# Kernel tuning notes

Hardware: AMD Instinct MI355X
Metric: run time of the kernel (lower is better)

The kernel has to match this reference:

```python
import jax, jax.numpy as jnp
import numpy as np

B, DIM, H, W = 8, 128, 64, 64
C, DI, N, R, K = DIM // 4, 2 * (DIM // 4), 16, 2, 4  # chunk dim, d_inner, d_state, dt_rank, n_dirs
L = H * W
EPS = 1e-5


def dwconv(x, w, b, dil):
    # x: [B,C,H,W]; w: [C,1,kh,kw] depthwise; torch padding='same' with dilation
    y = jax.lax.conv_general_dilated(
        x, w, window_strides=(1, 1), padding='SAME', rhs_dilation=(dil, dil),
        dimension_numbers=('NCHW', 'OIHW', 'NCHW'), feature_group_count=x.shape[1])
    return y + b[None, :, None, None]


def layernorm(x, w, b):
    mu = jnp.mean(x, -1, keepdims=True)
    var = jnp.var(x, -1, keepdims=True)
    return (x - mu) * jax.lax.rsqrt(var + EPS) * w + b


def axial_dw(x, mh_w, mh_b, mw_w, mw_b, c_w, c_b, dil):
    skip = x
    x = dwconv(x, mw_w, mw_b, dil)   # (1,7) kernel
    x = dwconv(x, mh_w, mh_b, dil)   # (7,1) kernel
    x = dwconv(x, c_w, c_b, dil)     # 3x3 kernel
    return x + skip


def ss2d(x, in_proj_w, conv_w, conv_b, x_proj_w, dt_proj_w, dt_proj_b,
         A_log, D, out_norm_w, out_norm_b, out_proj_w):
    # x: [B,H,W,C] channels-last (VMamba SS2D)
    b, h, w, _ = x.shape
    xz = jnp.einsum('bhwc,ec->bhwe', x, in_proj_w)          # [B,H,W,2*DI]
    xc, z = jnp.split(xz, 2, axis=-1)
    xc = xc.transpose(0, 3, 1, 2)                           # [B,DI,H,W]
    xc = jax.nn.silu(dwconv(xc, conv_w, conv_b, 1))
    l = h * w
    x_hw = xc.reshape(b, DI, l)
    x_wh = xc.transpose(0, 1, 3, 2).reshape(b, DI, l)
    xs = jnp.stack([x_hw, x_wh], 1)                         # [B,2,DI,L]
    xs = jnp.concatenate([xs, jnp.flip(xs, -1)], 1)         # [B,4,DI,L]
    x_dbl = jnp.einsum('bkdl,kcd->bkcl', xs, x_proj_w)      # c = R+2N
    dts, Bs, Cs = x_dbl[:, :, :R], x_dbl[:, :, R:R + N], x_dbl[:, :, R + N:]
    dts = jnp.einsum('bkrl,kdr->bkdl', dts, dt_proj_w)
    delta = jax.nn.softplus(dts + dt_proj_b[None, :, :, None])  # [B,4,DI,L]
    A = -jnp.exp(A_log)                                     # [4,DI,N]

    def step(hst, inp):
        u_t, dt_t, B_t, C_t = inp  # [B,4,DI],[B,4,DI],[B,4,N],[B,4,N]
        dA = jnp.exp(dt_t[..., None] * A)                   # [B,4,DI,N]
        hst = hst * dA + (dt_t * u_t)[..., None] * B_t[:, :, None, :]
        y = jnp.einsum('bkdn,bkn->bkd', hst, C_t)
        return hst, y

    u_l = jnp.moveaxis(xs, -1, 0)
    dt_l = jnp.moveaxis(delta, -1, 0)
    B_l = jnp.moveaxis(Bs, -1, 0)
    C_l = jnp.moveaxis(Cs, -1, 0)
    h0 = jnp.zeros((b, K, DI, N), xc.dtype)
    _, ys = jax.lax.scan(step, h0, (u_l, dt_l, B_l, C_l))   # [L,B,4,DI]
    out_y = jnp.moveaxis(ys, 0, -1) + D[None, :, :, None] * xs  # [B,4,DI,L]

    inv_y = jnp.flip(out_y[:, 2:4], -1)
    wh_y = out_y[:, 1].reshape(b, DI, w, h).transpose(0, 1, 3, 2).reshape(b, DI, l)
    invwh_y = inv_y[:, 1].reshape(b, DI, w, h).transpose(0, 1, 3, 2).reshape(b, DI, l)
    y = out_y[:, 0] + inv_y[:, 0] + wh_y + invwh_y          # [B,DI,L]
    y = y.transpose(0, 2, 1).reshape(b, h, w, DI)
    y = layernorm(y, out_norm_w, out_norm_b)
    y = y * jax.nn.silu(z)
    return jnp.einsum('bhwd,cd->bhwc', y, out_proj_w)


def setup_inputs() -> dict:
    key = jax.random.key(0)
    ks = iter(jax.random.split(key, 64))
    nrm = lambda s, sc=0.05: jax.random.normal(next(ks), s, jnp.float32) * sc
    inp = {'x': jax.random.normal(next(ks), (B, DIM, H, W), jnp.float32)}
    for i in (1, 2, 3):
        inp[f'dw{i}_mh_w'] = nrm((C, 1, 7, 1), 0.1); inp[f'dw{i}_mh_b'] = nrm((C,), 0.02)
        inp[f'dw{i}_mw_w'] = nrm((C, 1, 1, 7), 0.1); inp[f'dw{i}_mw_b'] = nrm((C,), 0.02)
        inp[f'dw{i}_c_w'] = nrm((C, 1, 3, 3), 0.1); inp[f'dw{i}_c_b'] = nrm((C,), 0.02)
    inp['ln_w'] = jnp.ones((C,)); inp['ln_b'] = jnp.zeros((C,))
    inp['in_proj_w'] = nrm((2 * DI, C))
    inp['conv_w'] = nrm((DI, 1, 3, 3), 0.1); inp['conv_b'] = nrm((DI,), 0.02)
    inp['x_proj_w'] = nrm((K, R + 2 * N, DI))
    inp['dt_proj_w'] = nrm((K, DI, R), 0.1)
    inp['dt_proj_b'] = nrm((K, DI), 0.02)
    inp['A_log'] = jax.random.uniform(next(ks), (K, DI, N), jnp.float32, 0.0, 2.0)
    inp['D'] = jnp.ones((K, DI), jnp.float32)
    inp['out_norm_w'] = jnp.ones((DI,)); inp['out_norm_b'] = jnp.zeros((DI,))
    inp['out_proj_w'] = nrm((C, DI))
    inp['bn_g'] = jnp.ones((DIM,)); inp['bn_b'] = jnp.zeros((DIM,))
    inp['bn_m'] = jnp.zeros((DIM,)); inp['bn_v'] = jnp.ones((DIM,))
    return inp


def reference(x, dw1_mh_w, dw1_mh_b, dw1_mw_w, dw1_mw_b, dw1_c_w, dw1_c_b,
              dw2_mh_w, dw2_mh_b, dw2_mw_w, dw2_mw_b, dw2_c_w, dw2_c_b,
              dw3_mh_w, dw3_mh_b, dw3_mw_w, dw3_mw_b, dw3_c_w, dw3_c_b,
              ln_w, ln_b, in_proj_w, conv_w, conv_b, x_proj_w, dt_proj_w, dt_proj_b,
              A_log, D, out_norm_w, out_norm_b, out_proj_w, bn_g, bn_b, bn_m, bn_v):
    def vss(xc):  # shared VSSBlock: [B,C,H,W] -> [B,C,H,W]
        t = xc.transpose(0, 2, 3, 1)
        t = t + ss2d(layernorm(t, ln_w, ln_b), in_proj_w, conv_w, conv_b, x_proj_w,
                     dt_proj_w, dt_proj_b, A_log, D, out_norm_w, out_norm_b, out_proj_w)
        return t.transpose(0, 3, 1, 2)

    x1, x2, x3, x4 = jnp.split(x, 4, axis=1)
    x1 = vss(axial_dw(x1, dw1_mh_w, dw1_mh_b, dw1_mw_w, dw1_mw_b, dw1_c_w, dw1_c_b, 1))
    x2 = vss(axial_dw(x2, dw2_mh_w, dw2_mh_b, dw2_mw_w, dw2_mw_b, dw2_c_w, dw2_c_b, 2))
    x3 = vss(axial_dw(x3, dw3_mh_w, dw3_mh_b, dw3_mw_w, dw3_mw_b, dw3_c_w, dw3_c_b, 3))
    xc = jnp.concatenate([x1, x2, x3, x4], axis=1)
    # BatchNorm2d in inference mode (running stats)
    y = (xc - bn_m[None, :, None, None]) * jax.lax.rsqrt(bn_v + EPS)[None, :, None, None]
    y = y * bn_g[None, :, None, None] + bn_b[None, :, None, None]
    return jax.nn.relu(y)
```

## Files before the change

kernel.cpp:

```cpp
#include <hip/hip_runtime.h>
#include <math.h>

#define LB __launch_bounds__(256)
#define LB512 __launch_bounds__(512)

#define LOG2E 1.44269504088896340736f
static __device__ __forceinline__ float silu_f(float x){ return x / (1.f + __expf(-x)); }
static __device__ __forceinline__ float softplus_f(float x){
    return (x > 20.f) ? x : __logf(1.f + __expf(x));
}

struct AxialArgs { const float* w[18]; };

__global__ LB void axial_kernel(const float* __restrict__ x, AxialArgs args,
    float* __restrict__ acc,
    const float* __restrict__ bn_g, const float* __restrict__ bn_b,
    const float* __restrict__ bn_m, const float* __restrict__ bn_v,
    float* __restrict__ out)
{
    __shared__ float s0[4096];
    __shared__ float s1[4096];
    if (blockIdx.x >= 768){
        const int gid = (blockIdx.x - 768)*256 + threadIdx.x;
        const int e = gid*4;
        const int l = e & 4095, bc = e >> 12;
        const int c = bc & 31, b = bc >> 5;
        const int ch = 96 + c;
        const size_t idx = ((size_t)b*128+ch)*4096 + l;
        float4 v = *(const float4*)&x[idx];
        const float sc = rsqrtf(bn_v[ch]+1e-5f)*bn_g[ch];
        const float mb = bn_m[ch], bbv = bn_b[ch];
        v.x = fmaxf((v.x-mb)*sc+bbv, 0.f);
        v.y = fmaxf((v.y-mb)*sc+bbv, 0.f);
        v.z = fmaxf((v.z-mb)*sc+bbv, 0.f);
        v.w = fmaxf((v.w-mb)*sc+bbv, 0.f);
        *(float4*)&out[idx] = v;
        return;
    }
    const int chunk = blockIdx.x >> 8;
    const int bc = blockIdx.x & 255;
    const int b = bc >> 5, c = bc & 31;
    const int dil = chunk + 1;
    const float* mh_w = args.w[chunk*6+0];
    const float* mh_b = args.w[chunk*6+1];
    const float* mw_w = args.w[chunk*6+2];
    const float* mw_b = args.w[chunk*6+3];
    const float* cw   = args.w[chunk*6+4];
    const float* cb   = args.w[chunk*6+5];
    const int tid = threadIdx.x;
    const float* xin = x + ((size_t)(b*128 + chunk*32 + c)) * 4096;
    float orig[16];
    #pragma unroll
    for (int kk=0;kk<16;++kk){ float v=xin[tid+kk*256]; orig[kk]=v; s0[tid+kk*256]=v; }
    __syncthreads();

    float w7[7];
    #pragma unroll
    for (int t=0;t<7;++t) w7[t]=mw_w[c*7+t];
    float bias = mw_b[c];
    float v[16];
    #pragma unroll
    for (int kk=0;kk<16;++kk){
        int p=tid+kk*256, i=p>>6, j=p&63;
        float s=bias;
        #pragma unroll
        for (int t=0;t<7;++t){ int jj=j+(t-3)*dil; if (jj>=0&&jj<64) s+=s0[i*64+jj]*w7[t]; }
        v[kk]=s;
    }
    #pragma unroll
    for (int kk=0;kk<16;++kk) s1[tid+kk*256]=v[kk];
    __syncthreads();

    #pragma unroll
    for (int t=0;t<7;++t) w7[t]=mh_w[c*7+t];
    bias = mh_b[c];
    #pragma unroll
    for (int kk=0;kk<16;++kk){
        int p=tid+kk*256, i=p>>6, j=p&63;
        float s=bias;
        #pragma unroll
        for (int t=0;t<7;++t){ int ii=i+(t-3)*dil; if (ii>=0&&ii<64) s+=s1[ii*64+j]*w7[t]; }
        v[kk]=s;
    }
    __syncthreads();
    #pragma unroll
    for (int kk=0;kk<16;++kk) s0[tid+kk*256]=v[kk];
    __syncthreads();

    float w9[9];
    #pragma unroll
    for (int t=0;t<9;++t) w9[t]=cw[c*9+t];
    bias = cb[c];
    float* aout = acc + (size_t)chunk*1048576 + ((size_t)(b*32+c))*4096;
    #pragma unroll
    for (int kk=0;kk<16;++kk){
        int p=tid+kk*256, i=p>>6, j=p&63;
        float s=bias;
        #pragma unroll
        for (int a=0;a<3;++a){
            int ii=i+(a-1)*dil; if (ii<0||ii>=64) continue;
            #pragma unroll
            for (int bb2=0;bb2<3;++bb2){
                int jj=j+(bb2-1)*dil; if (jj<0||jj>=64) continue;
                s += s0[ii*64+jj]*w9[a*3+bb2];
            }
        }
        aout[p] = s + orig[kk];
    }
}

__global__ LB512 void lnproj_kernel(const float* __restrict__ acc, int ch0, size_t cs,
    const float* __restrict__ ln_w, const float* __restrict__ ln_b,
    const float* __restrict__ in_proj_w,
    float* __restrict__ xc, float* __restrict__ z)
{
    __shared__ float s_a[32*65];
    const int cl = blockIdx.x >> 9;
    const int local = blockIdx.x & 511;
    const int chunk = ch0 + cl;
    const int b = local >> 6, lt = local & 63;
    const int l0 = lt*64;
    const int tid = threadIdx.x;
    const float* ab = acc + (size_t)chunk*1048576 + (size_t)b*32*4096 + l0;
    for (int i=tid;i<2048;i+=512){ int c=i>>6, j=i&63; s_a[c*65+j]=ab[(size_t)c*4096 + j]; }
    __syncthreads();
    const int l = tid & 63;
    const int g = __builtin_amdgcn_readfirstlane(tid >> 6);
    float v[32];
    float mu=0.f;
    #pragma unroll
    for (int c=0;c<32;++c){ v[c]=s_a[c*65+l]; mu+=v[c]; }
    mu *= (1.f/32.f);
    float var=0.f;
    #pragma unroll
    for (int c=0;c<32;++c){ float d2=v[c]-mu; var+=d2*d2; }
    var *= (1.f/32.f);
    float rs = rsqrtf(var+1e-5f);
    #pragma unroll
    for (int c=0;c<32;++c) v[c] = (v[c]-mu)*rs*ln_w[c] + ln_b[c];
    float* xcp = xc + (size_t)cl*cs + (size_t)b*64*4096 + l0 + l;
    float* zp  = z  + (size_t)cl*cs + (size_t)b*64*4096 + l0 + l;
    for (int e=g*16; e<g*16+16; ++e){
        const float* wr = in_proj_w + e*32;
        float s=0.f;
        #pragma unroll
        for (int c=0;c<32;++c) s += wr[c]*v[c];
        if (e<64) xcp[(size_t)e*4096]=s; else zp[(size_t)(e-64)*4096]=s;
    }
}

__global__ LB void conv3_kernel(const float* __restrict__ xc, size_t cs,
    const float* __restrict__ conv_w, const float* __restrict__ conv_b,
    float* __restrict__ xconv, float* __restrict__ xconvT)
{
    __shared__ float s0[4096];
    __shared__ float s1[64*65];
    const int cl = blockIdx.x >> 9;
    const int bd = blockIdx.x & 511;
    const int d = bd & 63;
    const int tid = threadIdx.x;
    const float* in = xc + (size_t)cl*cs + (size_t)bd*4096;
    #pragma unroll
    for (int kk=0;kk<16;++kk) s0[tid+kk*256]=in[tid+kk*256];
    __syncthreads();
    float w9[9];
    #pragma unroll
    for (int t=0;t<9;++t) w9[t]=conv_w[d*9+t];
    float bias = conv_b[d];
    float* outp = xconv + (size_t)cl*cs + (size_t)bd*4096;
    #pragma unroll
    for (int kk=0;kk<16;++kk){
        int p=tid+kk*256, i=p>>6, j=p&63;
        float s=bias;
        #pragma unroll
        for (int a=0;a<3;++a){
            int ii=i+a-1; if (ii<0||ii>=64) continue;
            #pragma unroll
            for (int bb2=0;bb2<3;++bb2){
                int jj=j+bb2-1; if (jj<0||jj>=64) continue;
                s += s0[ii*64+jj]*w9[a*3+bb2];
            }
        }
        s = silu_f(s);
        outp[p]=s;
        s1[i*65+j]=s;
    }
    __syncthreads();
    float* outT = xconvT + (size_t)cl*cs + (size_t)bd*4096;
    #pragma unroll
    for (int kk=0;kk<16;++kk){ int p=tid+kk*256; outT[p] = s1[(p&63)*65 + (p>>6)]; }
}

__global__ LB void projscan1_kernel(const float* __restrict__ xconv, const float* __restrict__ xconvT,
    size_t cs,
    const float* __restrict__ x_proj_w, const float* __restrict__ dt_proj_w,
    const float* __restrict__ dt_proj_b, const float* __restrict__ A_log,
    float* __restrict__ Bsb, float* __restrict__ Csb, float* __restrict__ dts_g,
    float* __restrict__ Ssum, float* __restrict__ hloc)
{
    __shared__ float s_x[64*65];
    __shared__ float s_dlt[64*65];
    __shared__ float s_B[64*17];
    __shared__ float s_C[64*17];
    __shared__ float s_dts[128];
    __shared__ float s_Spart[4][64];
    const int cl = blockIdx.x >> 11;
    const int blkL = blockIdx.x & 2047;
    const int g = blkL & 63, bk = blkL >> 6;
    const int k = bk & 3, b = bk >> 2;
    const int tid = threadIdx.x;
    const int t0 = g*64;
    const float* src = ((k & 1) ? xconvT : xconv) + (size_t)cl*cs;
    const float* sb = src + (size_t)b*64*4096;
    for (int i=tid;i<4096;i+=256){
        int d=i>>6, j=i&63;
        int col = (k&2) ? (4095-(t0+j)) : (t0+j);
        s_x[j*65+d] = sb[(size_t)d*4096 + col];
    }
    __syncthreads();

    {
        const int t = tid & 63;
        const int q = __builtin_amdgcn_readfirstlane(tid >> 6);
        const float* wp = x_proj_w + k*2176;
        float acc9[9];
        #pragma unroll
        for (int r=0;r<9;++r) acc9[r]=0.f;
        const int r0 = q*9;
        const int nr = (q==3)?7:9;
        for (int ch=0; ch<4; ++ch){
            float xv[16];
            #pragma unroll
            for (int i=0;i<16;++i) xv[i] = s_x[t*65 + ch*16 + i];
            #pragma unroll
            for (int r=0;r<9;++r){
                if (r < nr){
                    const float* wr = wp + (r0+r)*64 + ch*16;
                    float s=0.f;
                    #pragma unroll
                    for (int i=0;i<16;++i) s += wr[i]*xv[i];
                    acc9[r] += s;
                }
            }
        }
        #pragma unroll
        for (int r=0;r<9;++r){
            if (r<nr){
                int row = r0 + r;
                if (row < 2)       s_dts[t*2 + row]      = acc9[r];
                else if (row < 18) s_B[t*17 + (row-2)]   = acc9[r];
                else               s_C[t*17 + (row-18)]  = acc9[r];
            }
        }
    }
    __syncthreads();

    {
        float* BsbC = Bsb + (size_t)cl*cs;
        float* CsbC = Csb + (size_t)cl*cs;
        const size_t tb = (size_t)blkL*1024;
        for (int i=tid;i<1024;i+=256){
            int a = (i>>4)*17 + (i&15);
            BsbC[tb+i]=s_B[a]; CsbC[tb+i]=s_C[a];
        }
        if (tid<128) (dts_g + (size_t)cl*cs)[(size_t)blkL*128 + tid] = s_dts[tid];
    }
    {
        const int d_ = tid & 63, part = tid >> 6;
        const float w0 = dt_proj_w[k*128 + d_*2], w1 = dt_proj_w[k*128 + d_*2 + 1];
        const float bb = dt_proj_b[k*64 + d_];
        float Sp = 0.f;
        #pragma unroll
        for (int i=0;i<16;++i){
            const int t = part*16 + i;
            float dlt = softplus_f(s_dts[t*2]*w0 + s_dts[t*2+1]*w1 + bb);
            s_dlt[t*65 + d_] = dlt;
            Sp += dlt;
        }
        s_Spart[part][d_] = Sp;
    }
    __syncthreads();
    if (tid < 64){
        (Ssum + (size_t)cl*cs)[(size_t)blkL*64 + tid] =
            s_Spart[0][tid]+s_Spart[1][tid]+s_Spart[2][tid]+s_Spart[3][tid];
    }

    const int d = tid & 63;
    const int w = __builtin_amdgcn_readfirstlane(tid >> 6);
    float4 Av = *(const float4*)(A_log + ((size_t)(k*64+d)*16 + w*4));
    const float A0 = -__expf(Av.x)*LOG2E, A1 = -__expf(Av.y)*LOG2E,
                A2 = -__expf(Av.z)*LOG2E, A3 = -__expf(Av.w)*LOG2E;
    float h0=0,h1=0,h2=0,h3=0;
    #pragma unroll 4
    for (int t=0;t<64;++t){
        float dlt = s_dlt[t*65+d];
        float du  = dlt * s_x[t*65+d];
        float b0 = s_B[t*17 + w*4 + 0];
        float b1 = s_B[t*17 + w*4 + 1];
        float b2 = s_B[t*17 + w*4 + 2];
        float b3 = s_B[t*17 + w*4 + 3];
        h0 = h0*exp2f(dlt*A0) + du*b0;
        h1 = h1*exp2f(dlt*A1) + du*b1;
        h2 = h2*exp2f(dlt*A2) + du*b2;
        h3 = h3*exp2f(dlt*A3) + du*b3;
    }
    ((float4*)(hloc + (size_t)cl*cs))[(size_t)blkL*256 + d*4 + w] = make_float4(h0,h1,h2,h3);
}

__global__ LB void scan2_kernel(const float* __restrict__ Ssum, size_t cs,
    const float* __restrict__ hloc, const float* __restrict__ A_log,
    float* __restrict__ hin)
{
    const int cl = blockIdx.x >> 7;
    const int j = (blockIdx.x & 127)*256 + threadIdx.x;
    const int bk = j >> 10, dn = j & 1023;
    const int k = bk & 3, d = dn >> 4, n = dn & 15;
    const float* SsC = Ssum + (size_t)cl*cs;
    const float* hlC = hloc + (size_t)cl*cs;
    float* hinC = hin + (size_t)cl*cs;
    const float A = -__expf(A_log[(size_t)(k*64+d)*16 + n]) * LOG2E;
    float h = 0.f;
    for (int g=0; g<64; ++g){
        const size_t o = ((size_t)bk*64 + g)*1024 + dn;
        hinC[o] = h;
        float S = SsC[((size_t)bk*64 + g)*64 + d];
        h = exp2f(A*S)*h + hlC[o];
    }
}

__global__ LB void scan3_kernel(const float* __restrict__ xconv, const float* __restrict__ xconvT,
    size_t cs,
    const float* __restrict__ Bsb, const float* __restrict__ Csb,
    const float* __restrict__ dts_g,
    const float* __restrict__ dt_proj_w, const float* __restrict__ dt_proj_b,
    const float* __restrict__ A_log, const float* __restrict__ Dp,
    const float* __restrict__ hin, float* __restrict__ outy)
{
    __shared__ __align__(16) float s_B[4][1024];
    __shared__ __align__(16) float s_C[4][1024];
    __shared__ float s_dts[4][128];
    __shared__ float s_y[4][64*17];
    const int cl = blockIdx.x >> 9;
    const int w = threadIdx.x >> 6;
    const int lane = threadIdx.x & 63;
    const int tile = (blockIdx.x & 511)*4 + w;
    const int g = tile & 63, bk = tile >> 6;
    const int k = bk & 3, b = bk >> 2;

    {
        const float4* B4 = (const float4*)(Bsb + (size_t)cl*cs + (size_t)tile*1024);
        const float4* C4 = (const float4*)(Csb + (size_t)cl*cs + (size_t)tile*1024);
        float4* sB4 = (float4*)s_B[w];
        float4* sC4 = (float4*)s_C[w];
        #pragma unroll
        for (int qq=0;qq<4;++qq){ sB4[lane+64*qq]=B4[lane+64*qq]; sC4[lane+64*qq]=C4[lane+64*qq]; }
        const float* dtsC = dts_g + (size_t)cl*cs;
        s_dts[w][lane]      = dtsC[(size_t)tile*128 + lane];
        s_dts[w][lane+64]   = dtsC[(size_t)tile*128 + lane + 64];
    }
    const int d = lane;
    float A[16];
    {
        const float* Ab = A_log + (size_t)(k*64+d)*16;
        #pragma unroll
        for (int n=0;n<16;++n) A[n] = -__expf(Ab[n])*LOG2E;
    }
    float h[16];
    {
        const float4* hb = (const float4*)(hin + (size_t)cl*cs + (size_t)tile*1024 + d*16);
        #pragma unroll
        for (int qq=0;qq<4;++qq){
            float4 v=hb[qq];
            h[qq*4+0]=v.x; h[qq*4+1]=v.y; h[qq*4+2]=v.z; h[qq*4+3]=v.w;
        }
    }
    const float w0 = dt_proj_w[k*128 + d*2], w1 = dt_proj_w[k*128 + d*2 + 1];
    const float bb = dt_proj_b[k*64 + d];
    const float Dv = Dp[k*64 + d];
    const float* up = ((k&1)?xconvT:xconv) + (size_t)cl*cs + (size_t)(b*64+d)*4096;
    const float4* sB4 = (const float4*)s_B[w];
    const float4* sC4 = (const float4*)s_C[w];
    float* syw = s_y[w];
    float* obase = outy + (size_t)cl*cs + (size_t)(bk*64)*4096 + g*64;

    for (int t4=0; t4<16; ++t4){
        float u4[4];
        if (k & 2){
            float4 r = *(const float4*)(up + (4092 - g*64 - t4*4));
            u4[0]=r.w; u4[1]=r.z; u4[2]=r.y; u4[3]=r.x;
        } else {
            float4 r = *(const float4*)(up + g*64 + t4*4);
            u4[0]=r.x; u4[1]=r.y; u4[2]=r.z; u4[3]=r.w;
        }
        #pragma unroll
        for (int j=0;j<4;++j){
            const int t = t4*4 + j;
            float dt0 = s_dts[w][t*2], dt1 = s_dts[w][t*2+1];
            float dlt = softplus_f(dt0*w0 + dt1*w1 + bb);
            float du  = dlt * u4[j];
            float y = 0.f;
            #pragma unroll
            for (int qq=0;qq<4;++qq){
                float4 Bv = sB4[t*4+qq];
                float4 Cv = sC4[t*4+qq];
                h[qq*4+0] = h[qq*4+0]*exp2f(dlt*A[qq*4+0]) + du*Bv.x;
                h[qq*4+1] = h[qq*4+1]*exp2f(dlt*A[qq*4+1]) + du*Bv.y;
                h[qq*4+2] = h[qq*4+2]*exp2f(dlt*A[qq*4+2]) + du*Bv.z;
                h[qq*4+3] = h[qq*4+3]*exp2f(dlt*A[qq*4+3]) + du*Bv.w;
                y += h[qq*4+0]*Cv.x + h[qq*4+1]*Cv.y + h[qq*4+2]*Cv.z + h[qq*4+3]*Cv.w;
            }
            syw[d*17 + (t & 15)] = y + Dv*u4[j];
        }
        if ((t4 & 3) == 3){
            const int tb = t4 >> 2;
            #pragma unroll
            for (int qq=0;qq<16;++qq){
                int i = qq*64 + lane;
                int dd = i >> 4, jj = i & 15;
                obase[(size_t)dd*4096 + tb*16 + jj] = syw[dd*17 + jj];
            }
        }
    }
}

__global__ LB void reduce4_kernel(const float* __restrict__ outy, size_t cs,
                                  float* __restrict__ ysum)
{
    __shared__ float s1[64*65];
    __shared__ float s3[64*65];
    const int cl = blockIdx.x >> 9;
    const int local = blockIdx.x & 511;
    const int b = local >> 6, d = local & 63;
    const int tid = threadIdx.x;
    const float* oy = outy + (size_t)cl*cs;
    const float* o0 = oy + ((size_t)((b*4+0)*64 + d))*4096;
    const float* o1 = oy + ((size_t)((b*4+1)*64 + d))*4096;
    const float* o2 = oy + ((size_t)((b*4+2)*64 + d))*4096;
    const float* o3 = oy + ((size_t)((b*4+3)*64 + d))*4096;
    #pragma unroll
    for (int it=0; it<16; ++it){
        int p = tid + it*256;
        s1[(p>>6)*65 + (p&63)] = o1[p];
        s3[(p>>6)*65 + (p&63)] = o3[p];
    }
    __syncthreads();
    float* ys = ysum + (size_t)cl*cs + ((size_t)(b*64 + d))*4096;
    #pragma unroll
    for (int it=0; it<16; ++it){
        int p = tid + it*256;
        int i = p >> 6, j = p & 63;
        ys[p] = o0[p] + o2[4095-p] + s1[j*65 + i] + s3[(63-j)*65 + (63-i)];
    }
}

__global__ LB512 void combine_kernel(const float* __restrict__ ysum, int ch0, size_t cs,
    const float* __restrict__ z, const float* __restrict__ acc,
    const float* __restrict__ onw, const float* __restrict__ onb,
    const float* __restrict__ opw,
    const float* __restrict__ bn_g, const float* __restrict__ bn_b,
    const float* __restrict__ bn_m, const float* __restrict__ bn_v,
    float* __restrict__ out)
{
    __shared__ float s_red[2][8][64];
    __shared__ float s_y[64*65];
    const int cl = blockIdx.x >> 9;
    const int chunk = ch0 + cl;
    const int local = blockIdx.x & 511;
    const int b = local >> 6, lt = local & 63;
    const int l0 = lt*64;
    const int tid = threadIdx.x;
    const int l = tid & 63;
    const int g = __builtin_amdgcn_readfirstlane(tid >> 6);
    const float* ys = ysum + (size_t)cl*cs + (size_t)b*64*4096;
    const int lf = l0 + l;
    float y[8];
    float psum=0.f, psq=0.f;
    #pragma unroll
    for (int i=0;i<8;++i){
        int d = g*8+i;
        float vv = ys[(size_t)d*4096 + lf];
        y[i]=vv; psum+=vv; psq+=vv*vv;
    }
    s_red[0][g][l]=psum; s_red[1][g][l]=psq;
    __syncthreads();
    float mu=0.f, vsum=0.f;
    #pragma unroll
    for (int gg=0;gg<8;++gg){ mu += s_red[0][gg][l]; vsum += s_red[1][gg][l]; }
    mu *= (1.f/64.f);
    float var = vsum*(1.f/64.f) - mu*mu;
    float rs = rsqrtf(var + 1e-5f);
    const float* zp = z + (size_t)cl*cs + (size_t)b*64*4096 + lf;
    #pragma unroll
    for (int i=0;i<8;++i){
        int d = g*8+i;
        float t2 = (y[i]-mu)*rs*onw[d] + onb[d];
        float zv = zp[(size_t)d*4096];
        s_y[l*65 + d] = t2 * silu_f(zv);
    }
    __syncthreads();
    float a4[4] = {0.f,0.f,0.f,0.f};
    for (int d=0; d<64; ++d){
        float xval = s_y[l*65+d];
        #pragma unroll
        for (int j=0;j<4;++j) a4[j] += opw[(g*4+j)*64+d]*xval;
    }
    const float* ap = acc + (size_t)chunk*1048576 + (size_t)b*32*4096 + lf;
    #pragma unroll
    for (int j=0;j<4;++j){
        int c = g*4+j, ch = chunk*32 + c;
        float s = a4[j] + ap[(size_t)c*4096];
        float bnv = (s - bn_m[ch])*rsqrtf(bn_v[ch]+1e-5f)*bn_g[ch] + bn_b[ch];
        out[((size_t)b*128+ch)*4096 + lf] = fmaxf(bnv, 0.f);
    }
}

extern "C" void kernel_launch(void* const* d_in, const int* in_sizes, int n_in,
                              void* d_out, int out_size, void* d_ws, size_t ws_size,
                              hipStream_t stream) {
    const float* x         = (const float*)d_in[0];
    const float* ln_w      = (const float*)d_in[19];
    const float* ln_b      = (const float*)d_in[20];
    const float* in_proj_w = (const float*)d_in[21];
    const float* conv_w    = (const float*)d_in[22];
    const float* conv_b    = (const float*)d_in[23];
    const float* x_proj_w  = (const float*)d_in[24];
    const float* dt_proj_w = (const float*)d_in[25];
    const float* dt_proj_b = (const float*)d_in[26];
    const float* A_log     = (const float*)d_in[27];
    const float* Dp        = (const float*)d_in[28];
    const float* onw       = (const float*)d_in[29];
    const float* onb       = (const float*)d_in[30];
    const float* opw       = (const float*)d_in[31];
    const float* bn_g      = (const float*)d_in[32];
    const float* bn_b      = (const float*)d_in[33];
    const float* bn_m      = (const float*)d_in[34];
    const float* bn_v      = (const float*)d_in[35];
    float* out = (float*)d_out;

    const size_t F_OUTY = 0;
    const size_t F_XC   = 0;
    const size_t F_HLO  = 2097152;
    const size_t F_Z    = 8388608;
    const size_t F_XCV  = 10485760;
    const size_t F_XCVT = 12582912;
    const size_t F_BSB  = 14680064;
    const size_t F_CSB  = 16777216;
    const size_t F_DTS  = 18874368;
    const size_t F_SSUM = 19136512;
    const size_t F_HIN  = 19267584;
    const size_t CSF    = 21364736;

    float* ws = (float*)d_ws;
    float* acc  = ws;
    float* pool = acc + 3145728;

    const size_t ws_f = ws_size / sizeof(float);
    int nch_max = 1;
    if (ws_f >= 3145728 + 3*CSF) nch_max = 3;
    else if (ws_f >= 3145728 + 2*CSF) nch_max = 2;

    float* xc     = pool + F_XC;
    float* z      = pool + F_Z;
    float* xconv  = pool + F_XCV;
    float* xconvT = pool + F_XCVT;
    float* Bsb    = pool + F_BSB;
    float* Csb    = pool + F_CSB;
    float* dts_g  = pool + F_DTS;
    float* Ssum   = pool + F_SSUM;
    float* hlo    = pool + F_HLO;
    float* hin    = pool + F_HIN;
    float* outy   = pool + F_OUTY;
    float* ysum   = pool + F_XCV;

    AxialArgs aargs;
    for (int chunk=0; chunk<3; ++chunk)
        for (int jj=0; jj<6; ++jj)
            aargs.w[chunk*6+jj] = (const float*)d_in[1 + chunk*6 + jj];
    axial_kernel<<<768+1024, 256, 0, stream>>>(x, aargs, acc, bn_g, bn_b, bn_m, bn_v, out);

    int done = 0;
    while (done < 3){
        const int nch = (3 - done < nch_max) ? (3 - done) : nch_max;
        const size_t cs = (nch > 1) ? CSF : 0;
        const int ch0 = done;

        lnproj_kernel<<<nch*512, 512, 0, stream>>>(acc, ch0, cs, ln_w, ln_b, in_proj_w, xc, z);
        conv3_kernel<<<nch*512, 256, 0, stream>>>(xc, cs, conv_w, conv_b, xconv, xconvT);
        projscan1_kernel<<<nch*2048, 256, 0, stream>>>(xconv, xconvT, cs,
                                                       x_proj_w, dt_proj_w, dt_proj_b,
                                                       A_log, Bsb, Csb, dts_g, Ssum, hlo);
        scan2_kernel<<<nch*128, 256, 0, stream>>>(Ssum, cs, hlo, A_log, hin);
        scan3_kernel<<<nch*512, 256, 0, stream>>>(xconv, xconvT, cs, Bsb, Csb, dts_g,
                                                  dt_proj_w, dt_proj_b, A_log, Dp, hin, outy);
        reduce4_kernel<<<nch*512, 256, 0, stream>>>(outy, cs, ysum);
        combine_kernel<<<nch*512, 512, 0, stream>>>(ysum, ch0, cs, z, acc, onw, onb, opw,
                                                    bn_g, bn_b, bn_m, bn_v, out);
        done += nch;
    }
}
```

Baseline: 457.2 us.

## Restructure projscan1 to process four tiles per block with per-lane full-state scan

projscan1 now handles four time tiles per block, running the x_proj projection for each tile in turn. It then runs the local chunk scan with one wavefront per tile, where each lane holds all 16 state entries, in the same way as scan3. This drops the shared delta buffer and the cross-wave S reduction, and recomputes softplus inside the scan. The grid shrinks by a factor of four and projection work inside each block is serialized with extra barriers, which may cut parallelism and add register pressure. Minor float2/float4 vectorized loads are also applied in scan3.

```diff
diff --git a/kernel.cpp b/kernel.cpp
--- a/kernel.cpp
+++ b/kernel.cpp
@@ -199,112 +199,125 @@
     float* __restrict__ Ssum, float* __restrict__ hloc)
 {
     __shared__ float s_x[64*65];
-    __shared__ float s_dlt[64*65];
-    __shared__ float s_B[64*17];
-    __shared__ float s_C[64*17];
-    __shared__ float s_dts[128];
-    __shared__ float s_Spart[4][64];
-    const int cl = blockIdx.x >> 11;
-    const int blkL = blockIdx.x & 2047;
-    const int g = blkL & 63, bk = blkL >> 6;
-    const int k = bk & 3, b = bk >> 2;
+    __shared__ __align__(16) float s_Bt[4][1024];
+    __shared__ __align__(16) float s_Ct[1024];
+    __shared__ __align__(8)  float s_dts[4][128];
+    const int cl = blockIdx.x >> 9;
+    const int blk4 = blockIdx.x & 511;
     const int tid = threadIdx.x;
-    const int t0 = g*64;
-    const float* src = ((k & 1) ? xconvT : xconv) + (size_t)cl*cs;
-    const float* sb = src + (size_t)b*64*4096;
-    for (int i=tid;i<4096;i+=256){
-        int d=i>>6, j=i&63;
-        int col = (k&2) ? (4095-(t0+j)) : (t0+j);
-        s_x[j*65+d] = sb[(size_t)d*4096 + col];
-    }
-    __syncthreads();
-
-    {
-        const int t = tid & 63;
-        const int q = __builtin_amdgcn_readfirstlane(tid >> 6);
-        const float* wp = x_proj_w + k*2176;
-        float acc9[9];
-        #pragma unroll
-        for (int r=0;r<9;++r) acc9[r]=0.f;
-        const int r0 = q*9;
-        const int nr = (q==3)?7:9;
-        for (int ch=0; ch<4; ++ch){
-            float xv[16];
+
+    for (int r=0; r<4; ++r){
+        const int tile = blk4*4 + r;
+        const int g = tile & 63, bk = tile >> 6;
+        const int k = bk & 3, b = bk >> 2;
+        const int t0 = g*64;
+        const float* src = ((k & 1) ? xconvT : xconv) + (size_t)cl*cs;
+        const float* sb = src + (size_t)b*64*4096;
+        for (int i=tid;i<4096;i+=256){
+            int d=i>>6, j=i&63;
+            int col = (k&2) ? (4095-(t0+j)) : (t0+j);
+            s_x[j*65+d] = sb[(size_t)d*4096 + col];
+        }
+        __syncthreads();
+        {
+            const int t = tid & 63;
+            const int q = __builtin_amdgcn_readfirstlane(tid >> 6);
+            const float* wp = x_proj_w + k*2176;
+            float acc9[9];
             #pragma unroll
-            for (int i=0;i<16;++i) xv[i] = s_x[t*65 + ch*16 + i];
-            #pragma unroll
-            for (int r=0;r<9;++r){
-                if (r < nr){
-                    const float* wr = wp + (r0+r)*64 + ch*16;
-                    float s=0.f;
-                    #pragma unroll
-                    for (int i=0;i<16;++i) s += wr[i]*xv[i];
-                    acc9[r] += s;
+            for (int rr=0;rr<9;++rr) acc9[rr]=0.f;
+            const int r0 = q*9;
+            const int nr = (q==3)?7:9;
+            for (int ch=0; ch<4; ++ch){
+                float xv[16];
+                #pragma unroll
+                for (int i=0;i<16;++i) xv[i] = s_x[t*65 + ch*16 + i];
+                #pragma unroll
+                for (int rr=0;rr<9;++rr){
+                    if (rr < nr){
+                        const float* wr = wp + (r0+rr)*64 + ch*16;
+                        float s=0.f;
+                        #pragma unroll
+                        for (int i=0;i<16;++i) s += wr[i]*xv[i];
+                        acc9[rr] += s;
+                    }
                 }
             }
-        }
-        #pragma unroll
-        for (int r=0;r<9;++r){
-            if (r<nr){
-                int row = r0 + r;
-                if (row < 2)       s_dts[t*2 + row]      = acc9[r];
-                else if (row < 18) s_B[t*17 + (row-2)]   = acc9[r];
-                else               s_C[t*17 + (row-18)]  = acc9[r];
+            #pragma unroll
+            for (int rr=0;rr<9;++rr){
+                if (rr<nr){
+                    int row = r0 + rr;
+                    if (row < 2)       s_dts[r][t*2 + row]   = acc9[rr];
+                    else if (row < 18) s_Bt[r][t*16+(row-2)] = acc9[rr];
+                    else               s_Ct[t*16+(row-18)]   = acc9[rr];
+                }
             }
         }
-    }
-    __syncthreads();
-
+        __syncthreads();
+        {
+            float* BsbC = Bsb + (size_t)cl*cs;
+            float* CsbC = Csb + (size_t)cl*cs;
+            const size_t tb = (size_t)tile*1024;
+            for (int i=tid;i<1024;i+=256){ BsbC[tb+i]=s_Bt[r][i]; CsbC[tb+i]=s_Ct[i]; }
+            if (tid<128) (dts_g + (size_t)cl*cs)[(size_t)tile*128 + tid] = s_dts[r][tid];
+        }
+        __syncthreads();
+    }
+
+    const int w = tid >> 6;
+    const int d = tid & 63;
+    const int tile = blk4*4 + w;
+    const int g = tile & 63, bk = tile >> 6;
+    const int k = bk & 3, b = bk >> 2;
+    float A[16];
     {
-        float* BsbC = Bsb + (size_t)cl*cs;
-        float* CsbC = Csb + (size_t)cl*cs;
-        const size_t tb = (size_t)blkL*1024;
-        for (int i=tid;i<1024;i+=256){
-            int a = (i>>4)*17 + (i&15);
-            BsbC[tb+i]=s_B[a]; CsbC[tb+i]=s_C[a];
-        }
-        if (tid<128) (dts_g + (size_t)cl*cs)[(size_t)blkL*128 + tid] = s_dts[tid];
-    }
-    {
-        const int d_ = tid & 63, part = tid >> 6;
-        const float w0 = dt_proj_w[k*128 + d_*2], w1 = dt_proj_w[k*128 + d_*2 + 1];
-        const float bb = dt_proj_b[k*64 + d_];
-        float Sp = 0.f;
-        #pragma unroll
-        for (int i=0;i<16;++i){
-            const int t = part*16 + i;
-            float dlt = softplus_f(s_dts[t*2]*w0 + s_dts[t*2+1]*w1 + bb);
-            s_dlt[t*65 + d_] = dlt;
-            Sp += dlt;
-        }
-        s_Spart[part][d_] = Sp;
-    }
-    __syncthreads();
-    if (tid < 64){
-        (Ssum + (size_t)cl*cs)[(size_t)blkL*64 + tid] =
-            s_Spart[0][tid]+s_Spart[1][tid]+s_Spart[2][tid]+s_Spart[3][tid];
-    }
-
-    const int d = tid & 63;
-    const int w = __builtin_amdgcn_readfirstlane(tid >> 6);
-    float4 Av = *(const float4*)(A_log + ((size_t)(k*64+d)*16 + w*4));
-    const float A0 = -__expf(Av.x)*LOG2E, A1 = -__expf(Av.y)*LOG2E,
-                A2 = -__expf(Av.z)*LOG2E, A3 = -__expf(Av.w)*LOG2E;
-    float h0=0,h1=0,h2=0,h3=0;
-    #pragma unroll 4
-    for (int t=0;t<64;++t){
-        float dlt = s_dlt[t*65+d];
-        float du  = dlt * s_x[t*65+d];
-        float b0 = s_B[t*17 + w*4 + 0];
-        float b1 = s_B[t*17 + w*4 + 1];
-        float b2 = s_B[t*17 + w*4 + 2];
-        float b3 = s_B[t*17 + w*4 + 3];
-        h0 = h0*exp2f(dlt*A0) + du*b0;
-        h1 = h1*exp2f(dlt*A1) + du*b1;
-        h2 = h2*exp2f(dlt*A2) + du*b2;
-        h3 = h3*exp2f(dlt*A3) + du*b3;
-    }
-    ((float4*)(hloc + (size_t)cl*cs))[(size_t)blkL*256 + d*4 + w] = make_float4(h0,h1,h2,h3);
+        const float4* Ab = (const float4*)(A_log + (size_t)(k*64+d)*16);
+        #pragma unroll
+        for (int qq=0;qq<4;++qq){
+            float4 v = Ab[qq];
+            A[qq*4+0]=-__expf(v.x)*LOG2E; A[qq*4+1]=-__expf(v.y)*LOG2E;
+            A[qq*4+2]=-__expf(v.z)*LOG2E; A[qq*4+3]=-__expf(v.w)*LOG2E;
+        }
+    }
+    const float w0 = dt_proj_w[k*128 + d*2], w1 = dt_proj_w[k*128 + d*2 + 1];
+    const float bb = dt_proj_b[k*64 + d];
+    const float* up = (((k&1)?xconvT:xconv) + (size_t)cl*cs) + (size_t)(b*64+d)*4096;
+    const float4* sB4 = (const float4*)s_Bt[w];
+    float h[16];
+    #pragma unroll
+    for (int n=0;n<16;++n) h[n]=0.f;
+    float S = 0.f;
+    for (int t4=0; t4<16; ++t4){
+        float u4[4];
+        if (k & 2){
+            float4 rr = *(const float4*)(up + (4092 - g*64 - t4*4));
+            u4[0]=rr.w; u4[1]=rr.z; u4[2]=rr.y; u4[3]=rr.x;
+        } else {
+            float4 rr = *(const float4*)(up + g*64 + t4*4);
+            u4[0]=rr.x; u4[1]=rr.y; u4[2]=rr.z; u4[3]=rr.w;
+        }
+        #pragma unroll
+        for (int j=0;j<4;++j){
+            const int t = t4*4 + j;
+            float2 dtv = *(const float2*)&s_dts[w][t*2];
+            float dlt = softplus_f(dtv.x*w0 + dtv.y*w1 + bb);
+            S += dlt;
+            float du = dlt * u4[j];
+            #pragma unroll
+            for (int qq=0;qq<4;++qq){
+                float4 Bv = sB4[t*4+qq];
+                h[qq*4+0] = h[qq*4+0]*exp2f(dlt*A[qq*4+0]) + du*Bv.x;
+                h[qq*4+1] = h[qq*4+1]*exp2f(dlt*A[qq*4+1]) + du*Bv.y;
+                h[qq*4+2] = h[qq*4+2]*exp2f(dlt*A[qq*4+2]) + du*Bv.z;
+                h[qq*4+3] = h[qq*4+3]*exp2f(dlt*A[qq*4+3]) + du*Bv.w;
+            }
+        }
+    }
+    (Ssum + (size_t)cl*cs)[(size_t)tile*64 + d] = S;
+    float4* hb = (float4*)(hloc + (size_t)cl*cs) + (size_t)tile*256 + d*4;
+    #pragma unroll
+    for (int qq=0;qq<4;++qq)
+        hb[qq] = make_float4(h[qq*4+0],h[qq*4+1],h[qq*4+2],h[qq*4+3]);
 }
 
 __global__ LB void scan2_kernel(const float* __restrict__ Ssum, size_t cs,
@@ -338,7 +351,7 @@
 {
     __shared__ __align__(16) float s_B[4][1024];
     __shared__ __align__(16) float s_C[4][1024];
-    __shared__ float s_dts[4][128];
+    __shared__ __align__(8) float s_dts[4][128];
     __shared__ float s_y[4][64*17];
     const int cl = blockIdx.x >> 9;
     const int w = threadIdx.x >> 6;
@@ -361,9 +374,13 @@
     const int d = lane;
     float A[16];
     {
-        const float* Ab = A_log + (size_t)(k*64+d)*16;
-        #pragma unroll
-        for (int n=0;n<16;++n) A[n] = -__expf(Ab[n])*LOG2E;
+        const float4* Ab = (const float4*)(A_log + (size_t)(k*64+d)*16);
+        #pragma unroll
+        for (int qq=0;qq<4;++qq){
+            float4 v = Ab[qq];
+            A[qq*4+0]=-__expf(v.x)*LOG2E; A[qq*4+1]=-__expf(v.y)*LOG2E;
+            A[qq*4+2]=-__expf(v.z)*LOG2E; A[qq*4+3]=-__expf(v.w)*LOG2E;
+        }
     }
     float h[16];
     {
@@ -395,8 +412,8 @@
         #pragma unroll
         for (int j=0;j<4;++j){
             const int t = t4*4 + j;
-            float dt0 = s_dts[w][t*2], dt1 = s_dts[w][t*2+1];
-            float dlt = softplus_f(dt0*w0 + dt1*w1 + bb);
+            float2 dtv = *(const float2*)&s_dts[w][t*2];
+            float dlt = softplus_f(dtv.x*w0 + dtv.y*w1 + bb);
             float du  = dlt * u4[j];
             float y = 0.f;
             #pragma unroll
@@ -586,9 +603,9 @@
 
         lnproj_kernel<<<nch*512, 512, 0, stream>>>(acc, ch0, cs, ln_w, ln_b, in_proj_w, xc, z);
         conv3_kernel<<<nch*512, 256, 0, stream>>>(xc, cs, conv_w, conv_b, xconv, xconvT);
-        projscan1_kernel<<<nch*2048, 256, 0, stream>>>(xconv, xconvT, cs,
-                                                       x_proj_w, dt_proj_w, dt_proj_b,
-                                                       A_log, Bsb, Csb, dts_g, Ssum, hlo);
+        projscan1_kernel<<<nch*512, 256, 0, stream>>>(xconv, xconvT, cs,
+                                                      x_proj_w, dt_proj_w, dt_proj_b,
+                                                      A_log, Bsb, Csb, dts_g, Ssum, hlo);
         scan2_kernel<<<nch*128, 256, 0, stream>>>(Ssum, cs, hlo, A_log, hin);
         scan3_kernel<<<nch*512, 256, 0, stream>>>(xconv, xconvT, cs, Bsb, Csb, dts_g,
                                                   dt_proj_w, dt_proj_b, A_log, Dp, hin, outy);
```

Measured after the change: 489.8 us. +7.1%, slower.
